# Performance work log

Hardware: AMD Instinct MI355X
Metric: run time of the kernel (lower is better)

Reference implementation:

```python
import jax, jax.numpy as jnp
import numpy as np

B, T, D, H = 4096, 128, 32, 64

def _gru_layer(x, W_ih, W_hh, b_ih, b_hh):
    # x: [B, T, in]; W_ih: [3H, in]; W_hh: [3H, H]
    xg = jnp.einsum('bti,gi->btg', x, W_ih) + b_ih  # [B, T, 3H] input gates, one big GEMM
    def step(h, xg_t):
        gh = h @ W_hh.T + b_hh                      # [B, 3H]
        xr, xz, xn = jnp.split(xg_t, 3, axis=-1)
        hr, hz, hn = jnp.split(gh, 3, axis=-1)
        r = jax.nn.sigmoid(xr + hr)
        z = jax.nn.sigmoid(xz + hz)
        n = jnp.tanh(xn + r * hn)
        h_new = (1.0 - z) * n + z * h
        return h_new, h_new
    h0 = jnp.zeros((x.shape[0], W_hh.shape[1]), x.dtype)
    _, hs = jax.lax.scan(step, h0, jnp.swapaxes(xg, 0, 1))  # scan over time
    return jnp.swapaxes(hs, 0, 1)                   # [B, T, H]

def setup_inputs() -> dict:
    key = jax.random.key(0)
    ks = jax.random.split(key, 12)
    s = 0.1
    return {
        'x':     jax.random.normal(ks[0], (B, T, D), jnp.float32),
        'W_ih0': jax.random.normal(ks[1], (3 * H, D), jnp.float32) * s,
        'W_hh0': jax.random.normal(ks[2], (3 * H, H), jnp.float32) * s,
        'b_ih0': jax.random.normal(ks[3], (3 * H,), jnp.float32) * s,
        'b_hh0': jax.random.normal(ks[4], (3 * H,), jnp.float32) * s,
        'W_ih1': jax.random.normal(ks[5], (3 * H, H), jnp.float32) * s,
        'W_hh1': jax.random.normal(ks[6], (3 * H, H), jnp.float32) * s,
        'b_ih1': jax.random.normal(ks[7], (3 * H,), jnp.float32) * s,
        'b_hh1': jax.random.normal(ks[8], (3 * H,), jnp.float32) * s,
        'fc_w':  jax.random.normal(ks[9], (1, H), jnp.float32) * s,
        'fc_b':  jax.random.normal(ks[10], (1,), jnp.float32) * s,
    }

def reference(x, W_ih0, W_hh0, b_ih0, b_hh0, W_ih1, W_hh1, b_ih1, b_hh1, fc_w, fc_b):
    h1 = _gru_layer(x, W_ih0, W_hh0, b_ih0, b_hh0)   # layer 0
    h2 = _gru_layer(h1, W_ih1, W_hh1, b_ih1, b_hh1)  # layer 1
    last = h2[:, -1, :]                              # [B, H]
    out = last @ fc_w.T + fc_b                       # [B, 1]
    return jnp.squeeze(out, axis=-1)                 # [B]
```

## Files before the change

kernel.cpp:

```cpp
#include <hip/hip_runtime.h>

typedef _Float16 f16;
typedef f16 f16x8 __attribute__((ext_vector_type(8)));
typedef f16 f16x4 __attribute__((ext_vector_type(4)));
typedef __fp16 h16x2 __attribute__((ext_vector_type(2)));
typedef float f32x4 __attribute__((ext_vector_type(4)));
typedef float f32x2 __attribute__((ext_vector_type(2)));

#define MFMA16(A, B, C) __builtin_amdgcn_mfma_f32_16x16x32_f16((A), (B), (C), 0, 0, 0)

#define LGKM_DRAIN() asm volatile("s_waitcnt lgkmcnt(0)" ::: "memory")

__device__ __forceinline__ float E2(float x) {
#if __has_builtin(__builtin_amdgcn_exp2f)
  return __builtin_amdgcn_exp2f(x);
#else
  return __expf(x * 0.69314718056f);
#endif
}

__device__ __forceinline__ f16x8 cvt8(float4 a, float4 b) {
  union { h16x2 h[4]; f16x8 v; } u;
  u.h[0] = __builtin_amdgcn_cvt_pkrtz(a.x, a.y);
  u.h[1] = __builtin_amdgcn_cvt_pkrtz(a.z, a.w);
  u.h[2] = __builtin_amdgcn_cvt_pkrtz(b.x, b.y);
  u.h[3] = __builtin_amdgcn_cvt_pkrtz(b.z, b.w);
  return u.v;
}

__device__ __forceinline__ void wait2(volatile int* fl, int thrA, int thrB) {
  while (fl[0] < thrA || fl[1] < thrB) { }
}

__device__ __forceinline__ void gates_pair(f32x2 aR, f32x2 aZ, f32x2 aXN,
                                           f32x2 aHN, f32x2& hs) {
  const float K = -1.44269504f;
  f32x2 mR = aR * K;
  f32x2 mZ = aZ * K;
  f32x2 ea, eb;
  ea[0] = E2(mR[0]); ea[1] = E2(mR[1]);
  eb[0] = E2(mZ[0]); eb[1] = E2(mZ[1]);
  f32x2 pa = ea + 1.0f;
  f32x2 pb = eb + 1.0f;
  f32x2 prod = pa * pb;
  f32x2 inv;
  inv[0] = __builtin_amdgcn_rcpf(prod[0]);
  inv[1] = __builtin_amdgcn_rcpf(prod[1]);
  f32x2 rg = pb * inv;
  f32x2 zg = pa * inv;
  f32x2 y = rg * aHN + aXN;
  f32x2 my = y * (2.0f * K);
  f32x2 c;
  c[0] = E2(my[0]); c[1] = E2(my[1]);
  f32x2 num = 1.0f - c;
  f32x2 den = 1.0f + c;
  f32x2 rin;
  rin[0] = __builtin_amdgcn_rcpf(den[0]);
  rin[1] = __builtin_amdgcn_rcpf(den[1]);
  f32x2 ng = num * rin;
  hs = zg * (hs - ng) + ng;
}

__launch_bounds__(512, 2)
__global__ void gru_fused(const float* __restrict__ x,
                          const float* __restrict__ Wih0, const float* __restrict__ Whh0,
                          const float* __restrict__ bih0, const float* __restrict__ bhh0,
                          const float* __restrict__ Wih1, const float* __restrict__ Whh1,
                          const float* __restrict__ bih1, const float* __restrict__ bhh1,
                          const float* __restrict__ fcw, const float* __restrict__ fcb,
                          float* __restrict__ out) {
  __shared__ f16 H0[4][1024];
  __shared__ f16 H1[2][1024];
  __shared__ float red[4][16];
  __shared__ int flags[2];

  const int tid = threadIdx.x;
  const int wave = tid >> 6;
  const int lane = tid & 63;
  const int l15 = lane & 15;
  const int q = lane >> 4;
  const int wa = wave & 3;
  const bool isB = wave >= 4;
  const int b0 = blockIdx.x * 16;

  for (int i = tid; i < 4096; i += 512) ((f16*)H0)[i] = (f16)0.0f;
  for (int i = tid; i < 2048; i += 512) ((f16*)H1)[i] = (f16)0.0f;
  if (tid == 0) { flags[0] = 0; flags[1] = 0; }

  f16x8 wAx[3];
  f16x8 wAh[3][2];
  f16x8 wBx[3][2];
  f16x8 wBh[3][2];
  f32x4 bR, bZ, bXN, bHN;
  float fw[4] = {0.f, 0.f, 0.f, 0.f};

  if (!isB) {
#pragma unroll
    for (int g = 0; g < 3; ++g) {
      const int row = g * 64 + 16 * wa + l15;
      const float* p = Wih0 + row * 32 + q * 8;
      wAx[g] = cvt8(*(const float4*)p, *(const float4*)(p + 4));
#pragma unroll
      for (int kf = 0; kf < 2; ++kf) {
        const float* ph = Whh0 + row * 64 + kf * 32 + q * 8;
        wAh[g][kf] = cvt8(*(const float4*)ph, *(const float4*)(ph + 4));
      }
    }
#pragma unroll
    for (int r = 0; r < 4; ++r) {
      const int o = 16 * wa + 4 * q + r;
      bR[r] = bih0[o] + bhh0[o];
      bZ[r] = bih0[64 + o] + bhh0[64 + o];
      bXN[r] = bih0[128 + o];
      bHN[r] = bhh0[128 + o];
    }
  } else {
#pragma unroll
    for (int g = 0; g < 3; ++g) {
      const int row = g * 64 + 16 * wa + l15;
#pragma unroll
      for (int kf = 0; kf < 2; ++kf) {
        const float* p1 = Wih1 + row * 64 + kf * 32 + q * 8;
        wBx[g][kf] = cvt8(*(const float4*)p1, *(const float4*)(p1 + 4));
        const float* p2 = Whh1 + row * 64 + kf * 32 + q * 8;
        wBh[g][kf] = cvt8(*(const float4*)p2, *(const float4*)(p2 + 4));
      }
    }
#pragma unroll
    for (int r = 0; r < 4; ++r) {
      const int o = 16 * wa + 4 * q + r;
      bR[r] = bih1[o] + bhh1[o];
      bZ[r] = bih1[64 + o] + bhh1[64 + o];
      bXN[r] = bih1[128 + o];
      bHN[r] = bhh1[128 + o];
      fw[r] = fcw[o];
    }
  }
  const float fcb0 = fcb[0];

  f32x2 hsA = {0.f, 0.f}, hsB2 = {0.f, 0.f};

  const int wk0 = 16 * wa + 4 * q;
  const int widx = ((wk0 >> 3) * 16 + l15) * 8 + (wk0 & 7);

  __syncthreads();

  if (!isB) {
    const float* xbase = x + (size_t)(b0 + l15) * 4096 + q * 8;
    float4 xa0 = *(const float4*)(xbase +  0), xb0 = *(const float4*)(xbase +  4);
    float4 xa1 = *(const float4*)(xbase + 32), xb1 = *(const float4*)(xbase + 36);
    float4 xa2 = *(const float4*)(xbase + 64), xb2 = *(const float4*)(xbase + 68);
    float4 xa3 = *(const float4*)(xbase + 96), xb3 = *(const float4*)(xbase + 100);

    auto stepA = [&](int t, const f16* H0r, f16* H0w, float4& pxa, float4& pxb) {
      wait2(flags, 4 * t, 4 * t - 12);
      const f16x8 xf = cvt8(pxa, pxb);
      if (t + 4 < 128) {
        const float* xp = xbase + (t + 4) * 32;
        pxa = *(const float4*)xp;
        pxb = *(const float4*)(xp + 4);
      }
      const f16x8 h0f0 = *(const f16x8*)&H0r[lane * 8];
      const f16x8 h0f1 = *(const f16x8*)&H0r[512 + lane * 8];
      f32x4 aR = bR, aZ = bZ, aXN = bXN, aHN = bHN;
      aR = MFMA16(wAx[0], xf, aR);
      aZ = MFMA16(wAx[1], xf, aZ);
      aR = MFMA16(wAh[0][0], h0f0, aR);
      aZ = MFMA16(wAh[1][0], h0f0, aZ);
      aR = MFMA16(wAh[0][1], h0f1, aR);
      aZ = MFMA16(wAh[1][1], h0f1, aZ);
      aXN = MFMA16(wAx[2], xf, aXN);
      aHN = MFMA16(wAh[2][0], h0f0, aHN);
      aHN = MFMA16(wAh[2][1], h0f1, aHN);
      gates_pair(f32x2{aR[0], aR[1]}, f32x2{aZ[0], aZ[1]},
                 f32x2{aXN[0], aXN[1]}, f32x2{aHN[0], aHN[1]}, hsA);
      gates_pair(f32x2{aR[2], aR[3]}, f32x2{aZ[2], aZ[3]},
                 f32x2{aXN[2], aXN[3]}, f32x2{aHN[2], aHN[3]}, hsB2);
      union { h16x2 h2[2]; f16x4 v; } uw;
      uw.h2[0] = __builtin_amdgcn_cvt_pkrtz(hsA[0], hsA[1]);
      uw.h2[1] = __builtin_amdgcn_cvt_pkrtz(hsB2[0], hsB2[1]);
      *(f16x4*)&H0w[widx] = uw.v;
      LGKM_DRAIN();
      if (lane == 0) atomicAdd(&flags[0], 1);
    };

#pragma unroll 1
    for (int t = 0; t < 128; t += 4) {
      stepA(t,     &H0[3][0], &H0[0][0], xa0, xb0);
      stepA(t + 1, &H0[0][0], &H0[1][0], xa1, xb1);
      stepA(t + 2, &H0[1][0], &H0[2][0], xa2, xb2);
      stepA(t + 3, &H0[2][0], &H0[3][0], xa3, xb3);
    }
  } else {
    auto stepB = [&](int t, const f16* H0r, const f16* H1r, f16* H1w) {
      wait2(flags, 4 * t + 4, 4 * t);
      const f16x8 g0 = *(const f16x8*)&H0r[lane * 8];
      const f16x8 g1 = *(const f16x8*)&H0r[512 + lane * 8];
      const f16x8 h1f0 = *(const f16x8*)&H1r[lane * 8];
      const f16x8 h1f1 = *(const f16x8*)&H1r[512 + lane * 8];
      f32x4 aR = bR, aZ = bZ, aXN = bXN, aHN = bHN;
      aR = MFMA16(wBx[0][0], g0, aR);
      aZ = MFMA16(wBx[1][0], g0, aZ);
      aR = MFMA16(wBx[0][1], g1, aR);
      aZ = MFMA16(wBx[1][1], g1, aZ);
      aR = MFMA16(wBh[0][0], h1f0, aR);
      aZ = MFMA16(wBh[1][0], h1f0, aZ);
      aR = MFMA16(wBh[0][1], h1f1, aR);
      aZ = MFMA16(wBh[1][1], h1f1, aZ);
      aXN = MFMA16(wBx[2][0], g0, aXN);
      aXN = MFMA16(wBx[2][1], g1, aXN);
      aHN = MFMA16(wBh[2][0], h1f0, aHN);
      aHN = MFMA16(wBh[2][1], h1f1, aHN);
      gates_pair(f32x2{aR[0], aR[1]}, f32x2{aZ[0], aZ[1]},
                 f32x2{aXN[0], aXN[1]}, f32x2{aHN[0], aHN[1]}, hsA);
      gates_pair(f32x2{aR[2], aR[3]}, f32x2{aZ[2], aZ[3]},
                 f32x2{aXN[2], aXN[3]}, f32x2{aHN[2], aHN[3]}, hsB2);
      union { h16x2 h2[2]; f16x4 v; } uw;
      uw.h2[0] = __builtin_amdgcn_cvt_pkrtz(hsA[0], hsA[1]);
      uw.h2[1] = __builtin_amdgcn_cvt_pkrtz(hsB2[0], hsB2[1]);
      *(f16x4*)&H1w[widx] = uw.v;
      LGKM_DRAIN();
      if (lane == 0) atomicAdd(&flags[1], 1);
    };

#pragma unroll 1
    for (int t = 0; t < 128; t += 4) {
      stepB(t,     &H0[0][0], &H1[1][0], &H1[0][0]);
      stepB(t + 1, &H0[1][0], &H1[0][0], &H1[1][0]);
      stepB(t + 2, &H0[2][0], &H1[1][0], &H1[0][0]);
      stepB(t + 3, &H0[3][0], &H1[0][0], &H1[1][0]);
    }

    float partial = fw[0] * hsA[0] + fw[1] * hsA[1] + fw[2] * hsB2[0] + fw[3] * hsB2[1];
    partial += __shfl_down(partial, 16, 64);
    partial += __shfl_down(partial, 32, 64);
    if (lane < 16) red[wa][l15] = partial;
  }

  __syncthreads();
  if (tid < 16) out[b0 + tid] = red[0][tid] + red[1][tid] + red[2][tid] + red[3][tid] + fcb0;
}

extern "C" void kernel_launch(void* const* d_in, const int* in_sizes, int n_in,
                              void* d_out, int out_size, void* d_ws, size_t ws_size,
                              hipStream_t stream) {
  (void)in_sizes; (void)n_in; (void)out_size; (void)d_ws; (void)ws_size;
  const float* x    = (const float*)d_in[0];
  const float* Wih0 = (const float*)d_in[1];
  const float* Whh0 = (const float*)d_in[2];
  const float* bih0 = (const float*)d_in[3];
  const float* bhh0 = (const float*)d_in[4];
  const float* Wih1 = (const float*)d_in[5];
  const float* Whh1 = (const float*)d_in[6];
  const float* bih1 = (const float*)d_in[7];
  const float* bhh1 = (const float*)d_in[8];
  const float* fcw  = (const float*)d_in[9];
  const float* fcb  = (const float*)d_in[10];
  float* out = (float*)d_out;

  gru_fused<<<256, 512, 0, stream>>>(x, Wih0, Whh0, bih0, bhh0,
                                     Wih1, Whh1, bih1, bhh1, fcw, fcb, out);
}
```

Baseline: 197.9 us.

## Collapse each GRU layer into one wave with register-resident state and LDS ring

```diff
diff --git a/kernel.cpp b/kernel.cpp
--- a/kernel.cpp
+++ b/kernel.cpp
@@ -2,13 +2,11 @@
 
 typedef _Float16 f16;
 typedef f16 f16x8 __attribute__((ext_vector_type(8)));
-typedef f16 f16x4 __attribute__((ext_vector_type(4)));
 typedef __fp16 h16x2 __attribute__((ext_vector_type(2)));
 typedef float f32x4 __attribute__((ext_vector_type(4)));
 typedef float f32x2 __attribute__((ext_vector_type(2)));
 
 #define MFMA16(A, B, C) __builtin_amdgcn_mfma_f32_16x16x32_f16((A), (B), (C), 0, 0, 0)
-
 #define LGKM_DRAIN() asm volatile("s_waitcnt lgkmcnt(0)" ::: "memory")
 
 __device__ __forceinline__ float E2(float x) {
@@ -26,10 +24,6 @@
   u.h[2] = __builtin_amdgcn_cvt_pkrtz(b.x, b.y);
   u.h[3] = __builtin_amdgcn_cvt_pkrtz(b.z, b.w);
   return u.v;
-}
-
-__device__ __forceinline__ void wait2(volatile int* fl, int thrA, int thrB) {
-  while (fl[0] < thrA || fl[1] < thrB) { }
 }
 
 __device__ __forceinline__ void gates_pair(f32x2 aR, f32x2 aZ, f32x2 aXN,
@@ -61,7 +55,12 @@
   hs = zg * (hs - ng) + ng;
 }
 
-__launch_bounds__(512, 2)
+__device__ __forceinline__ void waitFlag(volatile int* f, int thr) {
+  while (*f < thr) { }
+  asm volatile("" ::: "memory");
+}
+
+__launch_bounds__(128, 1)
 __global__ void gru_fused(const float* __restrict__ x,
                           const float* __restrict__ Wih0, const float* __restrict__ Whh0,
                           const float* __restrict__ bih0, const float* __restrict__ bhh0,
@@ -69,176 +68,184 @@
                           const float* __restrict__ bih1, const float* __restrict__ bhh1,
                           const float* __restrict__ fcw, const float* __restrict__ fcb,
                           float* __restrict__ out) {
-  __shared__ f16 H0[4][1024];
-  __shared__ f16 H1[2][1024];
-  __shared__ float red[4][16];
-  __shared__ int flags[2];
+  __shared__ f16 RING[8][1024];
+  __shared__ int flagA;
+  __shared__ int flagB;
 
   const int tid = threadIdx.x;
-  const int wave = tid >> 6;
+  const bool isB = tid >= 64;
   const int lane = tid & 63;
   const int l15 = lane & 15;
   const int q = lane >> 4;
-  const int wa = wave & 3;
-  const bool isB = wave >= 4;
   const int b0 = blockIdx.x * 16;
 
-  for (int i = tid; i < 4096; i += 512) ((f16*)H0)[i] = (f16)0.0f;
-  for (int i = tid; i < 2048; i += 512) ((f16*)H1)[i] = (f16)0.0f;
-  if (tid == 0) { flags[0] = 0; flags[1] = 0; }
-
-  f16x8 wAx[3];
-  f16x8 wAh[3][2];
-  f16x8 wBx[3][2];
-  f16x8 wBh[3][2];
-  f32x4 bR, bZ, bXN, bHN;
-  float fw[4] = {0.f, 0.f, 0.f, 0.f};
-
-  if (!isB) {
-#pragma unroll
-    for (int g = 0; g < 3; ++g) {
-      const int row = g * 64 + 16 * wa + l15;
-      const float* p = Wih0 + row * 32 + q * 8;
-      wAx[g] = cvt8(*(const float4*)p, *(const float4*)(p + 4));
+  if (tid == 0) { flagA = 0; flagB = 0; }
+
+  f16x8 wX[3][4][2];
+  f16x8 wH[3][4][2];
+  f32x4 bR[4], bZ[4], bXN[4], bHN[4];
+  float fw[4][4];
+
+  const float* WihP = isB ? Wih1 : Wih0;
+  const float* WhhP = isB ? Whh1 : Whh0;
+  const float* bihP = isB ? bih1 : bih0;
+  const float* bhhP = isB ? bhh1 : bhh0;
+  const int xstride = isB ? 64 : 32;
+
+#pragma unroll
+  for (int g = 0; g < 3; ++g) {
+#pragma unroll
+    for (int T = 0; T < 4; ++T) {
+      const int row = g * 64 + 32 * (T >> 1) + 8 * (l15 >> 2) + 4 * (T & 1) + (l15 & 3);
+      {
+        const float* p = WihP + row * xstride + q * 8;
+        wX[g][T][0] = cvt8(*(const float4*)p, *(const float4*)(p + 4));
+        if (isB) {
+          const float* p1 = p + 32;
+          wX[g][T][1] = cvt8(*(const float4*)p1, *(const float4*)(p1 + 4));
+        }
+      }
 #pragma unroll
       for (int kf = 0; kf < 2; ++kf) {
-        const float* ph = Whh0 + row * 64 + kf * 32 + q * 8;
-        wAh[g][kf] = cvt8(*(const float4*)ph, *(const float4*)(ph + 4));
-      }
-    }
+        const float* ph = WhhP + row * 64 + kf * 32 + q * 8;
+        wH[g][T][kf] = cvt8(*(const float4*)ph, *(const float4*)(ph + 4));
+      }
+    }
+  }
+#pragma unroll
+  for (int T = 0; T < 4; ++T)
 #pragma unroll
     for (int r = 0; r < 4; ++r) {
-      const int o = 16 * wa + 4 * q + r;
-      bR[r] = bih0[o] + bhh0[o];
-      bZ[r] = bih0[64 + o] + bhh0[64 + o];
-      bXN[r] = bih0[128 + o];
-      bHN[r] = bhh0[128 + o];
-    }
-  } else {
-#pragma unroll
-    for (int g = 0; g < 3; ++g) {
-      const int row = g * 64 + 16 * wa + l15;
-#pragma unroll
-      for (int kf = 0; kf < 2; ++kf) {
-        const float* p1 = Wih1 + row * 64 + kf * 32 + q * 8;
-        wBx[g][kf] = cvt8(*(const float4*)p1, *(const float4*)(p1 + 4));
-        const float* p2 = Whh1 + row * 64 + kf * 32 + q * 8;
-        wBh[g][kf] = cvt8(*(const float4*)p2, *(const float4*)(p2 + 4));
-      }
-    }
-#pragma unroll
-    for (int r = 0; r < 4; ++r) {
-      const int o = 16 * wa + 4 * q + r;
-      bR[r] = bih1[o] + bhh1[o];
-      bZ[r] = bih1[64 + o] + bhh1[64 + o];
-      bXN[r] = bih1[128 + o];
-      bHN[r] = bhh1[128 + o];
-      fw[r] = fcw[o];
-    }
-  }
+      const int o = 32 * (T >> 1) + 8 * q + 4 * (T & 1) + r;
+      bR[T][r] = bihP[o] + bhhP[o];
+      bZ[T][r] = bihP[64 + o] + bhhP[64 + o];
+      bXN[T][r] = bihP[128 + o];
+      bHN[T][r] = bhhP[128 + o];
+      fw[T][r] = fcw[o];
+    }
   const float fcb0 = fcb[0];
 
-  f32x2 hsA = {0.f, 0.f}, hsB2 = {0.f, 0.f};
-
-  const int wk0 = 16 * wa + 4 * q;
-  const int widx = ((wk0 >> 3) * 16 + l15) * 8 + (wk0 & 7);
+  f32x2 hs01[4] = {{0.f,0.f},{0.f,0.f},{0.f,0.f},{0.f,0.f}};
+  f32x2 hs23[4] = {{0.f,0.f},{0.f,0.f},{0.f,0.f},{0.f,0.f}};
+  f16x8 hf0 = {}, hf1 = {};
 
   __syncthreads();
 
   if (!isB) {
     const float* xbase = x + (size_t)(b0 + l15) * 4096 + q * 8;
-    float4 xa0 = *(const float4*)(xbase +  0), xb0 = *(const float4*)(xbase +  4);
+    float4 xa0 = *(const float4*)xbase,        xb0 = *(const float4*)(xbase + 4);
     float4 xa1 = *(const float4*)(xbase + 32), xb1 = *(const float4*)(xbase + 36);
-    float4 xa2 = *(const float4*)(xbase + 64), xb2 = *(const float4*)(xbase + 68);
-    float4 xa3 = *(const float4*)(xbase + 96), xb3 = *(const float4*)(xbase + 100);
-
-    auto stepA = [&](int t, const f16* H0r, f16* H0w, float4& pxa, float4& pxb) {
-      wait2(flags, 4 * t, 4 * t - 12);
-      const f16x8 xf = cvt8(pxa, pxb);
-      if (t + 4 < 128) {
-        const float* xp = xbase + (t + 4) * 32;
-        pxa = *(const float4*)xp;
-        pxb = *(const float4*)(xp + 4);
-      }
-      const f16x8 h0f0 = *(const f16x8*)&H0r[lane * 8];
-      const f16x8 h0f1 = *(const f16x8*)&H0r[512 + lane * 8];
-      f32x4 aR = bR, aZ = bZ, aXN = bXN, aHN = bHN;
-      aR = MFMA16(wAx[0], xf, aR);
-      aZ = MFMA16(wAx[1], xf, aZ);
-      aR = MFMA16(wAh[0][0], h0f0, aR);
-      aZ = MFMA16(wAh[1][0], h0f0, aZ);
-      aR = MFMA16(wAh[0][1], h0f1, aR);
-      aZ = MFMA16(wAh[1][1], h0f1, aZ);
-      aXN = MFMA16(wAx[2], xf, aXN);
-      aHN = MFMA16(wAh[2][0], h0f0, aHN);
-      aHN = MFMA16(wAh[2][1], h0f1, aHN);
-      gates_pair(f32x2{aR[0], aR[1]}, f32x2{aZ[0], aZ[1]},
-                 f32x2{aXN[0], aXN[1]}, f32x2{aHN[0], aHN[1]}, hsA);
-      gates_pair(f32x2{aR[2], aR[3]}, f32x2{aZ[2], aZ[3]},
-                 f32x2{aXN[2], aXN[3]}, f32x2{aHN[2], aHN[3]}, hsB2);
-      union { h16x2 h2[2]; f16x4 v; } uw;
-      uw.h2[0] = __builtin_amdgcn_cvt_pkrtz(hsA[0], hsA[1]);
-      uw.h2[1] = __builtin_amdgcn_cvt_pkrtz(hsB2[0], hsB2[1]);
-      *(f16x4*)&H0w[widx] = uw.v;
+
+#pragma unroll 1
+    for (int tb = 0; tb < 128; tb += 4) {
+      if (tb >= 8) waitFlag(&flagB, tb - 4);
+#pragma unroll
+      for (int s = 0; s < 4; ++s) {
+        const int t = tb + s;
+        const float4 cxa = (s & 1) ? xa1 : xa0;
+        const float4 cxb = (s & 1) ? xb1 : xb0;
+        if (t + 2 < 128) {
+          const float* xp = xbase + (t + 2) * 32;
+          if (s & 1) { xa1 = *(const float4*)xp; xb1 = *(const float4*)(xp + 4); }
+          else       { xa0 = *(const float4*)xp; xb0 = *(const float4*)(xp + 4); }
+        }
+        const f16x8 xf = cvt8(cxa, cxb);
+#pragma unroll
+        for (int T = 0; T < 4; ++T) {
+          f32x4 aR  = MFMA16(wX[0][T][0], xf, bR[T]);
+          f32x4 aZ  = MFMA16(wX[1][T][0], xf, bZ[T]);
+          f32x4 aXN = MFMA16(wX[2][T][0], xf, bXN[T]);
+          f32x4 aHN = MFMA16(wH[2][T][0], hf0, bHN[T]);
+          aR  = MFMA16(wH[0][T][0], hf0, aR);
+          aZ  = MFMA16(wH[1][T][0], hf0, aZ);
+          aR  = MFMA16(wH[0][T][1], hf1, aR);
+          aZ  = MFMA16(wH[1][T][1], hf1, aZ);
+          aHN = MFMA16(wH[2][T][1], hf1, aHN);
+          gates_pair(f32x2{aR[0], aR[1]}, f32x2{aZ[0], aZ[1]},
+                     f32x2{aXN[0], aXN[1]}, f32x2{aHN[0], aHN[1]}, hs01[T]);
+          gates_pair(f32x2{aR[2], aR[3]}, f32x2{aZ[2], aZ[3]},
+                     f32x2{aXN[2], aXN[3]}, f32x2{aHN[2], aHN[3]}, hs23[T]);
+        }
+        union { h16x2 h2[4]; f16x8 v; } u0, u1;
+        u0.h2[0] = __builtin_amdgcn_cvt_pkrtz(hs01[0][0], hs01[0][1]);
+        u0.h2[1] = __builtin_amdgcn_cvt_pkrtz(hs23[0][0], hs23[0][1]);
+        u0.h2[2] = __builtin_amdgcn_cvt_pkrtz(hs01[1][0], hs01[1][1]);
+        u0.h2[3] = __builtin_amdgcn_cvt_pkrtz(hs23[1][0], hs23[1][1]);
+        u1.h2[0] = __builtin_amdgcn_cvt_pkrtz(hs01[2][0], hs01[2][1]);
+        u1.h2[1] = __builtin_amdgcn_cvt_pkrtz(hs23[2][0], hs23[2][1]);
+        u1.h2[2] = __builtin_amdgcn_cvt_pkrtz(hs01[3][0], hs01[3][1]);
+        u1.h2[3] = __builtin_amdgcn_cvt_pkrtz(hs23[3][0], hs23[3][1]);
+        hf0 = u0.v; hf1 = u1.v;
+        f16* slot = &RING[t & 7][0];
+        *(f16x8*)&slot[lane * 8] = hf0;
+        *(f16x8*)&slot[512 + lane * 8] = hf1;
+      }
       LGKM_DRAIN();
-      if (lane == 0) atomicAdd(&flags[0], 1);
-    };
-
+      if (lane == 0) *(volatile int*)&flagA = tb + 4;
+    }
+  } else {
+    f16x8 gA0, gA1, gB0, gB1;
 #pragma unroll 1
-    for (int t = 0; t < 128; t += 4) {
-      stepA(t,     &H0[3][0], &H0[0][0], xa0, xb0);
-      stepA(t + 1, &H0[0][0], &H0[1][0], xa1, xb1);
-      stepA(t + 2, &H0[1][0], &H0[2][0], xa2, xb2);
-      stepA(t + 3, &H0[2][0], &H0[3][0], xa3, xb3);
-    }
-  } else {
-    auto stepB = [&](int t, const f16* H0r, const f16* H1r, f16* H1w) {
-      wait2(flags, 4 * t + 4, 4 * t);
-      const f16x8 g0 = *(const f16x8*)&H0r[lane * 8];
-      const f16x8 g1 = *(const f16x8*)&H0r[512 + lane * 8];
-      const f16x8 h1f0 = *(const f16x8*)&H1r[lane * 8];
-      const f16x8 h1f1 = *(const f16x8*)&H1r[512 + lane * 8];
-      f32x4 aR = bR, aZ = bZ, aXN = bXN, aHN = bHN;
-      aR = MFMA16(wBx[0][0], g0, aR);
-      aZ = MFMA16(wBx[1][0], g0, aZ);
-      aR = MFMA16(wBx[0][1], g1, aR);
-      aZ = MFMA16(wBx[1][1], g1, aZ);
-      aR = MFMA16(wBh[0][0], h1f0, aR);
-      aZ = MFMA16(wBh[1][0], h1f0, aZ);
-      aR = MFMA16(wBh[0][1], h1f1, aR);
-      aZ = MFMA16(wBh[1][1], h1f1, aZ);
-      aXN = MFMA16(wBx[2][0], g0, aXN);
-      aXN = MFMA16(wBx[2][1], g1, aXN);
-      aHN = MFMA16(wBh[2][0], h1f0, aHN);
-      aHN = MFMA16(wBh[2][1], h1f1, aHN);
-      gates_pair(f32x2{aR[0], aR[1]}, f32x2{aZ[0], aZ[1]},
-                 f32x2{aXN[0], aXN[1]}, f32x2{aHN[0], aHN[1]}, hsA);
-      gates_pair(f32x2{aR[2], aR[3]}, f32x2{aZ[2], aZ[3]},
-                 f32x2{aXN[2], aXN[3]}, f32x2{aHN[2], aHN[3]}, hsB2);
-      union { h16x2 h2[2]; f16x4 v; } uw;
-      uw.h2[0] = __builtin_amdgcn_cvt_pkrtz(hsA[0], hsA[1]);
-      uw.h2[1] = __builtin_amdgcn_cvt_pkrtz(hsB2[0], hsB2[1]);
-      *(f16x4*)&H1w[widx] = uw.v;
+    for (int tb = 0; tb < 128; tb += 4) {
+      waitFlag(&flagA, tb + 4);
+      {
+        const f16* slot = &RING[tb & 7][0];
+        gA0 = *(const f16x8*)&slot[lane * 8];
+        gA1 = *(const f16x8*)&slot[512 + lane * 8];
+      }
+#pragma unroll
+      for (int s = 0; s < 4; ++s) {
+        const int t = tb + s;
+        const f16x8 g0 = (s & 1) ? gB0 : gA0;
+        const f16x8 g1 = (s & 1) ? gB1 : gA1;
+        if (s < 3) {
+          const f16* slot = &RING[(t + 1) & 7][0];
+          if (s & 1) { gA0 = *(const f16x8*)&slot[lane * 8]; gA1 = *(const f16x8*)&slot[512 + lane * 8]; }
+          else       { gB0 = *(const f16x8*)&slot[lane * 8]; gB1 = *(const f16x8*)&slot[512 + lane * 8]; }
+        }
+#pragma unroll
+        for (int T = 0; T < 4; ++T) {
+          f32x4 aR  = MFMA16(wX[0][T][0], g0, bR[T]);
+          f32x4 aZ  = MFMA16(wX[1][T][0], g0, bZ[T]);
+          f32x4 aXN = MFMA16(wX[2][T][0], g0, bXN[T]);
+          f32x4 aHN = MFMA16(wH[2][T][0], hf0, bHN[T]);
+          aR  = MFMA16(wX[0][T][1], g1, aR);
+          aZ  = MFMA16(wX[1][T][1], g1, aZ);
+          aXN = MFMA16(wX[2][T][1], g1, aXN);
+          aHN = MFMA16(wH[2][T][1], hf1, aHN);
+          aR  = MFMA16(wH[0][T][0], hf0, aR);
+          aZ  = MFMA16(wH[1][T][0], hf0, aZ);
+          aR  = MFMA16(wH[0][T][1], hf1, aR);
+          aZ  = MFMA16(wH[1][T][1], hf1, aZ);
+          gates_pair(f32x2{aR[0], aR[1]}, f32x2{aZ[0], aZ[1]},
+                     f32x2{aXN[0], aXN[1]}, f32x2{aHN[0], aHN[1]}, hs01[T]);
+          gates_pair(f32x2{aR[2], aR[3]}, f32x2{aZ[2], aZ[3]},
+                     f32x2{aXN[2], aXN[3]}, f32x2{aHN[2], aHN[3]}, hs23[T]);
+        }
+        union { h16x2 h2[4]; f16x8 v; } u0, u1;
+        u0.h2[0] = __builtin_amdgcn_cvt_pkrtz(hs01[0][0], hs01[0][1]);
+        u0.h2[1] = __builtin_amdgcn_cvt_pkrtz(hs23[0][0], hs23[0][1]);
+        u0.h2[2] = __builtin_amdgcn_cvt_pkrtz(hs01[1][0], hs01[1][1]);
+        u0.h2[3] = __builtin_amdgcn_cvt_pkrtz(hs23[1][0], hs23[1][1]);
+        u1.h2[0] = __builtin_amdgcn_cvt_pkrtz(hs01[2][0], hs01[2][1]);
+        u1.h2[1] = __builtin_amdgcn_cvt_pkrtz(hs23[2][0], hs23[2][1]);
+        u1.h2[2] = __builtin_amdgcn_cvt_pkrtz(hs01[3][0], hs01[3][1]);
+        u1.h2[3] = __builtin_amdgcn_cvt_pkrtz(hs23[3][0], hs23[3][1]);
+        hf0 = u0.v; hf1 = u1.v;
+      }
       LGKM_DRAIN();
-      if (lane == 0) atomicAdd(&flags[1], 1);
-    };
-
-#pragma unroll 1
-    for (int t = 0; t < 128; t += 4) {
-      stepB(t,     &H0[0][0], &H1[1][0], &H1[0][0]);
-      stepB(t + 1, &H0[1][0], &H1[0][0], &H1[1][0]);
-      stepB(t + 2, &H0[2][0], &H1[1][0], &H1[0][0]);
-      stepB(t + 3, &H0[3][0], &H1[0][0], &H1[1][0]);
-    }
-
-    float partial = fw[0] * hsA[0] + fw[1] * hsA[1] + fw[2] * hsB2[0] + fw[3] * hsB2[1];
+      if (lane == 0) *(volatile int*)&flagB = tb + 4;
+    }
+
+    float partial = 0.f;
+#pragma unroll
+    for (int T = 0; T < 4; ++T)
+      partial += fw[T][0] * hs01[T][0] + fw[T][1] * hs01[T][1] +
+                 fw[T][2] * hs23[T][0] + fw[T][3] * hs23[T][1];
     partial += __shfl_down(partial, 16, 64);
     partial += __shfl_down(partial, 32, 64);
-    if (lane < 16) red[wa][l15] = partial;
+    if (lane < 16) out[b0 + lane] = partial + fcb0;
   }
-
-  __syncthreads();
-  if (tid < 16) out[b0 + tid] = red[0][tid] + red[1][tid] + red[2][tid] + red[3][tid] + fcb0;
 }
 
 extern "C" void kernel_launch(void* const* d_in, const int* in_sizes, int n_in,
@@ -258,6 +265,6 @@
   const float* fcb  = (const float*)d_in[10];
   float* out = (float*)d_out;
 
-  gru_fused<<<256, 512, 0, stream>>>(x, Wih0, Whh0, bih0, bhh0,
+  gru_fused<<<256, 128, 0, stream>>>(x, Wih0, Whh0, bih0, bhh0,
                                      Wih1, Whh1, bih1, bhh1, fcw, fcb, out);
 }
```

New measurement: 236.3 us. 19.4% more time.
